# Kernel tuning notes

Hardware: AMD Instinct MI355X
Metric: run time of the kernel (lower is better)

Reference implementation:

```python
import math
import jax, jax.numpy as jnp
import numpy as np

B, T, N_EMBD, N_HEAD = 1, 16384, 1024, 1
N_ITERS = 30


def setup_inputs() -> dict:
    key = jax.random.key(0)
    kx, kw = jax.random.split(key)
    x = jax.random.normal(kx, (B, T, N_EMBD), dtype=jnp.float32)
    W = jax.random.normal(kw, (2 * N_EMBD + 1, N_EMBD), dtype=jnp.float32) * 0.02
    alpha = jnp.asarray(1.0, dtype=jnp.float32)  # nn.Parameter init
    beta = jnp.asarray(5.0, dtype=jnp.float32)   # nn.Parameter init
    return {"x": x, "W": W, "alpha": alpha, "beta": beta}


def _forward(x, W, alpha, beta):
    Bv, Tv, C = x.shape
    hd = C // N_HEAD
    qkv = x @ W.T                                            # (B,T,2C+1)
    q, k, v = qkv[..., :C], qkv[..., C:2 * C], qkv[..., 2 * C:]
    kh = k.reshape(Bv, Tv, N_HEAD, hd).transpose(0, 2, 1, 3)  # (B,H,T,hd)
    vh = v.reshape(Bv, Tv, N_HEAD, 1).transpose(0, 2, 1, 3)   # (B,H,T,1)
    q_last = q[:, -1].reshape(Bv, N_HEAD, hd)                 # last-token query
    scale = 0.001 / math.sqrt(hd)
    # Only the last query row of the causal attention matrix is consumed;
    # it attends all T keys (causal mask is all-ones on the last row).
    att = jnp.einsum('bhd,bhtd->bht', q_last, kh) * scale     # (B,H,T)
    att = att.at[:, :, -1].set(-jnp.inf)                      # exclude self key
    idx = jnp.arange(Tv)
    counts = (Tv - 1 - idx).astype(att.dtype)                 # distance from end

    def step(carry, _):
        a, b, k_old, done, p = carry
        kk = 2.0 * (a + b) / a                                # truncated window k = 2/p
        window = jnp.ceil(kk)
        mask = idx >= (Tv - window)                           # last `window` keys
        p_new = jax.nn.softmax(jnp.where(mask, att, -jnp.inf), axis=-1)
        bu = jnp.einsum('bht,t->', p_new, counts)             # beta_update (B=H=1 -> scalar)
        a_new, b_new = a + 1.0, b + bu
        done_new = done | (kk > Tv) | (kk < k_old)            # torch break conditions
        k_old_new = jax.lax.stop_gradient(kk)                 # k_old = k.detach()
        keep = lambda old, new: jnp.where(done, old, new)     # freeze after break
        return (keep(a, a_new), keep(b, b_new), keep(k_old, k_old_new),
                done_new, keep(p, p_new)), None

    init = (alpha.astype(att.dtype), beta.astype(att.dtype),
            jnp.asarray(0.0, att.dtype), jnp.asarray(False), jnp.zeros_like(att))
    (_, _, _, _, p), _ = jax.lax.scan(step, init, None, length=N_ITERS)
    # p is zero outside the final window, so the full-length contraction equals
    # att @ v[:, :, -window:, :].
    y = jnp.einsum('bht,bhtd->bhd', p, vh)
    return y.reshape(Bv, 1, 1)


def reference(x, W, alpha, beta):
    return _forward(x, W, alpha, beta)
```

## Files before the change

### kernel.cpp

```cpp
#include <hip/hip_runtime.h>
#include <math.h>

#define T_LEN 16384
#define C_DIM 1024
#define TAIL  256
#define SCAN_ITERS 30
#define NBLK 128
#define NTHR 512
#define ROWS_PER_BLK 8
#define ATT_PER_BLK  (TAIL / NBLK)

__global__ __launch_bounds__(NTHR)
void k_fused(const float* __restrict__ x, const float* __restrict__ W,
             const float* __restrict__ alpha_p, const float* __restrict__ beta_p,
             unsigned int* __restrict__ cnt, float* __restrict__ partials,
             float* __restrict__ att, float* __restrict__ v,
             float* __restrict__ out) {
    const int tid = threadIdx.x, lane = tid & 63, wid = tid >> 6;
    const int blk = blockIdx.x;

    __shared__ float q_sh[ROWS_PER_BLK];
    __shared__ float w_sh[C_DIM];
    __shared__ float redA[8], redV[8];
    __shared__ float red4[4];
    __shared__ float totZ[4], totC[4], totV[4];
    __shared__ float sZ[TAIL], sV[TAIL], sBU[TAIL];
    __shared__ int   last_sh;

    {
        const float4* xl = (const float4*)(x + (size_t)(T_LEN - 1) * C_DIM);
        const int i = blk * ROWS_PER_BLK + wid;
        const float4* wq = (const float4*)(W + (size_t)i * C_DIM);
        float acc = 0.f;
#pragma unroll
        for (int it = 0; it < 4; ++it) {
            float4 a = wq[lane + 64 * it];
            float4 b = xl[lane + 64 * it];
            acc += a.x * b.x + a.y * b.y + a.z * b.z + a.w * b.w;
        }
#pragma unroll
        for (int off = 32; off > 0; off >>= 1) acc += __shfl_down(acc, off, 64);
        if (lane == 0) q_sh[wid] = acc;
        __syncthreads();

        const float* Wk = W + (size_t)C_DIM * C_DIM;
        float2 p2 = make_float2(0.f, 0.f);
#pragma unroll
        for (int r = 0; r < ROWS_PER_BLK; ++r) {
            int ir = blk * ROWS_PER_BLK + r;
            float2 wkv = ((const float2*)(Wk + (size_t)ir * C_DIM))[tid];
            float qv = q_sh[r];
            p2.x += qv * wkv.x; p2.y += qv * wkv.y;
        }
        ((float2*)(partials + (size_t)blk * C_DIM))[tid] = p2;
    }

    __syncthreads();
    if (tid == 0) {
        __threadfence();
        atomicAdd(&cnt[0], 1u);
        while (__hip_atomic_load(&cnt[0], __ATOMIC_ACQUIRE,
                                 __HIP_MEMORY_SCOPE_AGENT) < NBLK) { }
    }
    __syncthreads();
    __threadfence();

    {
        float2 a2 = make_float2(0.f, 0.f);
        for (int b = 0; b < NBLK; ++b) {
            float2 p = ((const float2*)(partials + (size_t)b * C_DIM))[tid];
            a2.x += p.x; a2.y += p.y;
        }
        w_sh[2 * tid]     = a2.x;
        w_sh[2 * tid + 1] = a2.y;
        __syncthreads();

        const int r = wid >> 2, qt = wid & 3;
        const int gw = blk * ATT_PER_BLK + r;
        const int t  = T_LEN - TAIL + gw;
        const float4* xr  = (const float4*)(x + (size_t)t * C_DIM);
        const float4* ws4 = (const float4*)w_sh;
        const float4* wv  = (const float4*)(W + (size_t)(2 * C_DIM) * C_DIM);
        const int idx = qt * 64 + lane;
        float4 a  = xr[idx];
        float4 e  = ws4[idx];
        float4 bv = wv[idx];
        float accA = a.x * e.x  + a.y * e.y  + a.z * e.z  + a.w * e.w;
        float accV = a.x * bv.x + a.y * bv.y + a.z * bv.z + a.w * bv.w;
#pragma unroll
        for (int off = 32; off > 0; off >>= 1) {
            accA += __shfl_down(accA, off, 64);
            accV += __shfl_down(accV, off, 64);
        }
        if (lane == 0) { redA[wid] = accA; redV[wid] = accV; }
        __syncthreads();
        if (tid < ATT_PER_BLK) {
            float A = redA[4 * tid] + redA[4 * tid + 1] + redA[4 * tid + 2] + redA[4 * tid + 3];
            float V = redV[4 * tid] + redV[4 * tid + 1] + redV[4 * tid + 2] + redV[4 * tid + 3];
            int gw2 = blk * ATT_PER_BLK + tid;
            int t2  = T_LEN - TAIL + gw2;
            const float scale = (float)(0.001 / 32.0);
            att[gw2] = (t2 == T_LEN - 1) ? -INFINITY : A * scale;
            v[gw2]   = V;
        }
    }

    __syncthreads();
    if (tid == 0) {
        __threadfence();
        unsigned int ticket = atomicAdd(&cnt[1], 1u);
        last_sh = (ticket == NBLK - 1);
    }
    __syncthreads();
    if (!last_sh) return;
    __threadfence();

    const int u = TAIL - 1 - tid;
    float av = -INFINITY, vv = 0.f;
    if (tid < TAIL) { av = att[u]; vv = v[u]; }

    float m = av;
#pragma unroll
    for (int off = 32; off > 0; off >>= 1) m = fmaxf(m, __shfl_xor(m, off, 64));
    if (lane == 0 && wid < 4) red4[wid] = m;
    __syncthreads();
    m = fmaxf(fmaxf(red4[0], red4[1]), fmaxf(red4[2], red4[3]));

    float e = (tid < TAIL) ? expf(av - m) : 0.f;
    float c = e * (float)(TAIL - 1 - u);
    float w = e * vv;

    float pz = e, pc = c, pw = w;
#pragma unroll
    for (int off = 1; off < 64; off <<= 1) {
        float tz = __shfl_up(pz, off, 64);
        float tc = __shfl_up(pc, off, 64);
        float tw = __shfl_up(pw, off, 64);
        if (lane >= off) { pz += tz; pc += tc; pw += tw; }
    }
    if (lane == 63 && wid < 4) { totZ[wid] = pz; totC[wid] = pc; totV[wid] = pw; }
    __syncthreads();
    if (tid < TAIL) {
        float az = 0.f, ac = 0.f, aw = 0.f;
        for (int w2 = 0; w2 < wid; ++w2) { az += totZ[w2]; ac += totC[w2]; aw += totV[w2]; }
        float Zu = pz + az;
        sZ[u]  = Zu;
        sV[u]  = pw + aw;
        sBU[u] = (pc + ac) / Zu;
    }
    __syncthreads();

    if (tid == 0) {
        float a = alpha_p[0], b = beta_p[0], k_old = 0.f;
        int f_start = 0;
        for (int it = 0; it < SCAN_ITERS; ++it) {
            float kk = 2.0f * (a + b) / a;
            float wf = ceilf(kk);
            int start;
            if (wf >= (float)TAIL) start = 0;
            else { int win = (int)wf; start = TAIL - win; if (start < 0) start = 0; }

            float bu = sBU[start];
            f_start = start;
            bool done_next = (kk > (float)T_LEN) || (kk < k_old);
            k_old = kk;
            a += 1.0f;
            b += bu;
            if (done_next) break;
        }
        out[0] = sV[f_start] / sZ[f_start];
    }
}

extern "C" void kernel_launch(void* const* d_in, const int* in_sizes, int n_in,
                              void* d_out, int out_size, void* d_ws, size_t ws_size,
                              hipStream_t stream) {
    const float* x     = (const float*)d_in[0];
    const float* W     = (const float*)d_in[1];
    const float* alpha = (const float*)d_in[2];
    const float* beta  = (const float*)d_in[3];

    unsigned int* cnt = (unsigned int*)d_ws;
    float* ws         = (float*)d_ws;
    float* partials   = ws + 16;
    float* att        = partials + (size_t)NBLK * C_DIM;
    float* v          = att + TAIL;
    float* outp       = (float*)d_out;

    hipMemsetAsync(cnt, 0, 2 * sizeof(unsigned int), stream);
    k_fused<<<NBLK, NTHR, 0, stream>>>(x, W, alpha, beta, cnt,
                                       partials, att, v, outp);
}
```

Measured before the change: 133.9 us.

## Double grid size and distribute partial-sum reduction across blocks with extra grid barrier

Grid grows from 128 to 256 blocks, each handling 4 query rows (split across two half-waves) and one tail attention row. The reduction of per-block partials into the effective key vector, which every block used to repeat over all partials, is now split across 64 blocks and written to a shared buffer, followed by a second grid-wide spin barrier. Spin-waits use relaxed loads with s_sleep. This is meant to cut redundant partials reading and spread the q and W_k load over more CUs, at the cost of an extra global barrier and of relying on all 256 blocks being co-resident.

```diff
diff --git a/kernel.cpp b/kernel.cpp
--- a/kernel.cpp
+++ b/kernel.cpp
@@ -5,22 +5,23 @@
 #define C_DIM 1024
 #define TAIL  256
 #define SCAN_ITERS 30
-#define NBLK 128
+#define NBLK 256
 #define NTHR 512
-#define ROWS_PER_BLK 8
-#define ATT_PER_BLK  (TAIL / NBLK)
+#define ROWS_PER_BLK 4
+#define NRED 64
 
 __global__ __launch_bounds__(NTHR)
 void k_fused(const float* __restrict__ x, const float* __restrict__ W,
              const float* __restrict__ alpha_p, const float* __restrict__ beta_p,
-             unsigned int* __restrict__ cnt, float* __restrict__ partials,
+             unsigned int* __restrict__ cnt, float* __restrict__ w_eff,
              float* __restrict__ att, float* __restrict__ v,
-             float* __restrict__ out) {
+             float* __restrict__ partials, float* __restrict__ out) {
     const int tid = threadIdx.x, lane = tid & 63, wid = tid >> 6;
     const int blk = blockIdx.x;
 
+    __shared__ float qp[8];
     __shared__ float q_sh[ROWS_PER_BLK];
-    __shared__ float w_sh[C_DIM];
+    __shared__ float red2[8 * 16];
     __shared__ float redA[8], redV[8];
     __shared__ float red4[4];
     __shared__ float totZ[4], totC[4], totV[4];
@@ -28,28 +29,32 @@
     __shared__ int   last_sh;
 
     {
+        const int r = wid & 3, h = wid >> 2;
+        const int i = blk * ROWS_PER_BLK + r;
         const float4* xl = (const float4*)(x + (size_t)(T_LEN - 1) * C_DIM);
-        const int i = blk * ROWS_PER_BLK + wid;
         const float4* wq = (const float4*)(W + (size_t)i * C_DIM);
         float acc = 0.f;
 #pragma unroll
-        for (int it = 0; it < 4; ++it) {
-            float4 a = wq[lane + 64 * it];
-            float4 b = xl[lane + 64 * it];
+        for (int it = 0; it < 2; ++it) {
+            int idx = h * 128 + it * 64 + lane;
+            float4 a = wq[idx];
+            float4 b = xl[idx];
             acc += a.x * b.x + a.y * b.y + a.z * b.z + a.w * b.w;
         }
 #pragma unroll
         for (int off = 32; off > 0; off >>= 1) acc += __shfl_down(acc, off, 64);
-        if (lane == 0) q_sh[wid] = acc;
+        if (lane == 0) qp[wid] = acc;
+        __syncthreads();
+        if (tid < ROWS_PER_BLK) q_sh[tid] = qp[tid] + qp[tid + 4];
         __syncthreads();
 
         const float* Wk = W + (size_t)C_DIM * C_DIM;
         float2 p2 = make_float2(0.f, 0.f);
 #pragma unroll
-        for (int r = 0; r < ROWS_PER_BLK; ++r) {
-            int ir = blk * ROWS_PER_BLK + r;
+        for (int r2 = 0; r2 < ROWS_PER_BLK; ++r2) {
+            int ir = blk * ROWS_PER_BLK + r2;
             float2 wkv = ((const float2*)(Wk + (size_t)ir * C_DIM))[tid];
-            float qv = q_sh[r];
+            float qv = q_sh[r2];
             p2.x += qv * wkv.x; p2.y += qv * wkv.y;
         }
         ((float2*)(partials + (size_t)blk * C_DIM))[tid] = p2;
@@ -59,34 +64,53 @@
     if (tid == 0) {
         __threadfence();
         atomicAdd(&cnt[0], 1u);
-        while (__hip_atomic_load(&cnt[0], __ATOMIC_ACQUIRE,
-                                 __HIP_MEMORY_SCOPE_AGENT) < NBLK) { }
+        while (__hip_atomic_load(&cnt[0], __ATOMIC_RELAXED,
+                                 __HIP_MEMORY_SCOPE_AGENT) < NBLK)
+            __builtin_amdgcn_s_sleep(2);
     }
     __syncthreads();
     __threadfence();
 
+    if (blk < NRED) {
+        const int cl = tid & 15, rt = tid >> 4;
+        const int c = blk * 16 + cl;
+        float s = 0.f;
+#pragma unroll
+        for (int rr = 0; rr < 8; ++rr)
+            s += partials[(size_t)(rt + 32 * rr) * C_DIM + c];
+        s += __shfl_down(s, 32, 64);
+        s += __shfl_down(s, 16, 64);
+        if ((lane >> 4) == 0) red2[wid * 16 + cl] = s;
+        __syncthreads();
+        if (tid < 16) {
+            float t2 = 0.f;
+#pragma unroll
+            for (int w2 = 0; w2 < 8; ++w2) t2 += red2[w2 * 16 + tid];
+            w_eff[blk * 16 + tid] = t2;
+        }
+        __syncthreads();
+    }
+
+    if (tid == 0) {
+        __threadfence();
+        atomicAdd(&cnt[1], 1u);
+        while (__hip_atomic_load(&cnt[1], __ATOMIC_RELAXED,
+                                 __HIP_MEMORY_SCOPE_AGENT) < NBLK)
+            __builtin_amdgcn_s_sleep(2);
+    }
+    __syncthreads();
+    __threadfence();
+
     {
-        float2 a2 = make_float2(0.f, 0.f);
-        for (int b = 0; b < NBLK; ++b) {
-            float2 p = ((const float2*)(partials + (size_t)b * C_DIM))[tid];
-            a2.x += p.x; a2.y += p.y;
-        }
-        w_sh[2 * tid]     = a2.x;
-        w_sh[2 * tid + 1] = a2.y;
-        __syncthreads();
-
-        const int r = wid >> 2, qt = wid & 3;
-        const int gw = blk * ATT_PER_BLK + r;
-        const int t  = T_LEN - TAIL + gw;
-        const float4* xr  = (const float4*)(x + (size_t)t * C_DIM);
-        const float4* ws4 = (const float4*)w_sh;
-        const float4* wv  = (const float4*)(W + (size_t)(2 * C_DIM) * C_DIM);
-        const int idx = qt * 64 + lane;
-        float4 a  = xr[idx];
-        float4 e  = ws4[idx];
-        float4 bv = wv[idx];
-        float accA = a.x * e.x  + a.y * e.y  + a.z * e.z  + a.w * e.w;
-        float accV = a.x * bv.x + a.y * bv.y + a.z * bv.z + a.w * bv.w;
+        const int t = T_LEN - TAIL + blk;
+        const float2* xr  = (const float2*)(x + (size_t)t * C_DIM);
+        const float2* we2 = (const float2*)w_eff;
+        const float2* wv2 = (const float2*)(W + (size_t)(2 * C_DIM) * C_DIM);
+        float2 a  = xr[tid];
+        float2 e  = we2[tid];
+        float2 bv = wv2[tid];
+        float accA = a.x * e.x  + a.y * e.y;
+        float accV = a.x * bv.x + a.y * bv.y;
 #pragma unroll
         for (int off = 32; off > 0; off >>= 1) {
             accA += __shfl_down(accA, off, 64);
@@ -94,21 +118,20 @@
         }
         if (lane == 0) { redA[wid] = accA; redV[wid] = accV; }
         __syncthreads();
-        if (tid < ATT_PER_BLK) {
-            float A = redA[4 * tid] + redA[4 * tid + 1] + redA[4 * tid + 2] + redA[4 * tid + 3];
-            float V = redV[4 * tid] + redV[4 * tid + 1] + redV[4 * tid + 2] + redV[4 * tid + 3];
-            int gw2 = blk * ATT_PER_BLK + tid;
-            int t2  = T_LEN - TAIL + gw2;
+        if (tid == 0) {
+            float A = 0.f, V = 0.f;
+#pragma unroll
+            for (int w2 = 0; w2 < 8; ++w2) { A += redA[w2]; V += redV[w2]; }
             const float scale = (float)(0.001 / 32.0);
-            att[gw2] = (t2 == T_LEN - 1) ? -INFINITY : A * scale;
-            v[gw2]   = V;
+            att[blk] = (t == T_LEN - 1) ? -INFINITY : A * scale;
+            v[blk]   = V;
         }
     }
 
     __syncthreads();
     if (tid == 0) {
         __threadfence();
-        unsigned int ticket = atomicAdd(&cnt[1], 1u);
+        unsigned int ticket = atomicAdd(&cnt[2], 1u);
         last_sh = (ticket == NBLK - 1);
     }
     __syncthreads();
@@ -180,14 +203,15 @@
     const float* alpha = (const float*)d_in[2];
     const float* beta  = (const float*)d_in[3];
 
+    float* ws         = (float*)d_ws;
     unsigned int* cnt = (unsigned int*)d_ws;
-    float* ws         = (float*)d_ws;
-    float* partials   = ws + 16;
-    float* att        = partials + (size_t)NBLK * C_DIM;
+    float* w_eff      = ws + 16;
+    float* att        = w_eff + C_DIM;
     float* v          = att + TAIL;
+    float* partials   = v + TAIL;
     float* outp       = (float*)d_out;
 
-    hipMemsetAsync(cnt, 0, 2 * sizeof(unsigned int), stream);
+    hipMemsetAsync(cnt, 0, 4 * sizeof(unsigned int), stream);
     k_fused<<<NBLK, NTHR, 0, stream>>>(x, W, alpha, beta, cnt,
-                                       partials, att, v, outp);
+                                       w_eff, att, v, partials, outp);
 }
```

Result: slower. 191.4 us (+42.9%).

## Split fused kernel into three launches replacing grid-wide spin barrier

Applied to the files above, without the earlier changes.

The single fused kernel with a software grid barrier is replaced by three kernels: a partial q·Wk projection, a column reduction of partials across 64 blocks, and an att/v kernel that finishes the scan in the last block. The counter reset moves into the reduction kernel, so the separate memset launch goes away. This is meant to remove the spin-wait barrier and the serial 128-way partial reduction that every block repeated. In exchange it adds kernel launch boundaries, and the partial buffer grows to 256 rows.

```diff
diff --git a/kernel.cpp b/kernel.cpp
--- a/kernel.cpp
+++ b/kernel.cpp
@@ -5,86 +5,89 @@
 #define C_DIM 1024
 #define TAIL  256
 #define SCAN_ITERS 30
-#define NBLK 128
-#define NTHR 512
-#define ROWS_PER_BLK 8
-#define ATT_PER_BLK  (TAIL / NBLK)
 
-__global__ __launch_bounds__(NTHR)
-void k_fused(const float* __restrict__ x, const float* __restrict__ W,
-             const float* __restrict__ alpha_p, const float* __restrict__ beta_p,
-             unsigned int* __restrict__ cnt, float* __restrict__ partials,
-             float* __restrict__ att, float* __restrict__ v,
-             float* __restrict__ out) {
+
+__global__ __launch_bounds__(256)
+void k_qw(const float* __restrict__ x, const float* __restrict__ W,
+          float* __restrict__ partials) {
     const int tid = threadIdx.x, lane = tid & 63, wid = tid >> 6;
     const int blk = blockIdx.x;
+    __shared__ float q_sh[4];
 
-    __shared__ float q_sh[ROWS_PER_BLK];
-    __shared__ float w_sh[C_DIM];
-    __shared__ float redA[8], redV[8];
+    const float4* xl = (const float4*)(x + (size_t)(T_LEN - 1) * C_DIM);
+    const int row = blk * 4 + wid;
+    const float4* wq = (const float4*)(W + (size_t)row * C_DIM);
+    float acc = 0.f;
+#pragma unroll
+    for (int it = 0; it < 4; ++it) {
+        int idx = lane + 64 * it;
+        float4 a = wq[idx];
+        float4 b = xl[idx];
+        acc += a.x * b.x + a.y * b.y + a.z * b.z + a.w * b.w;
+    }
+#pragma unroll
+    for (int off = 32; off > 0; off >>= 1) acc += __shfl_down(acc, off, 64);
+    if (lane == 0) q_sh[wid] = acc;
+    __syncthreads();
+
+    const float* Wk = W + (size_t)C_DIM * C_DIM;
+    float4 p4 = make_float4(0.f, 0.f, 0.f, 0.f);
+#pragma unroll
+    for (int r = 0; r < 4; ++r) {
+        int ir = blk * 4 + r;
+        float4 wkv = ((const float4*)(Wk + (size_t)ir * C_DIM))[tid];
+        float qv = q_sh[r];
+        p4.x += qv * wkv.x; p4.y += qv * wkv.y;
+        p4.z += qv * wkv.z; p4.w += qv * wkv.w;
+    }
+    ((float4*)(partials + (size_t)blk * C_DIM))[tid] = p4;
+}
+
+__global__ __launch_bounds__(256)
+void k_red(const float* __restrict__ partials, float* __restrict__ w_eff,
+           unsigned int* __restrict__ cnt) {
+    const int tid = threadIdx.x, blk = blockIdx.x;
+    if (blk == 0 && tid == 0) cnt[0] = 0;
+    __shared__ float sh[16][17];
+    const int cl = tid & 15, seg = tid >> 4;
+    const int col = blk * 16 + cl;
+    float s = 0.f;
+#pragma unroll
+    for (int r = 0; r < 16; ++r)
+        s += partials[(size_t)(seg * 16 + r) * C_DIM + col];
+    sh[seg][cl] = s;
+    __syncthreads();
+    if (tid < 16) {
+        float t2 = 0.f;
+#pragma unroll
+        for (int g = 0; g < 16; ++g) t2 += sh[g][tid];
+        w_eff[blk * 16 + tid] = t2;
+    }
+}
+
+__global__ __launch_bounds__(256)
+void k_attv(const float* __restrict__ x, const float* __restrict__ W,
+            const float* __restrict__ w_eff,
+            const float* __restrict__ alpha_p, const float* __restrict__ beta_p,
+            unsigned int* __restrict__ cnt,
+            float* __restrict__ att, float* __restrict__ v,
+            float* __restrict__ out) {
+    const int tid = threadIdx.x, lane = tid & 63, wid = tid >> 6;
+    const int blk = blockIdx.x;
+    __shared__ float redA[4], redV[4];
     __shared__ float red4[4];
     __shared__ float totZ[4], totC[4], totV[4];
     __shared__ float sZ[TAIL], sV[TAIL], sBU[TAIL];
     __shared__ int   last_sh;
 
     {
-        const float4* xl = (const float4*)(x + (size_t)(T_LEN - 1) * C_DIM);
-        const int i = blk * ROWS_PER_BLK + wid;
-        const float4* wq = (const float4*)(W + (size_t)i * C_DIM);
-        float acc = 0.f;
-#pragma unroll
-        for (int it = 0; it < 4; ++it) {
-            float4 a = wq[lane + 64 * it];
-            float4 b = xl[lane + 64 * it];
-            acc += a.x * b.x + a.y * b.y + a.z * b.z + a.w * b.w;
-        }
-#pragma unroll
-        for (int off = 32; off > 0; off >>= 1) acc += __shfl_down(acc, off, 64);
-        if (lane == 0) q_sh[wid] = acc;
-        __syncthreads();
-
-        const float* Wk = W + (size_t)C_DIM * C_DIM;
-        float2 p2 = make_float2(0.f, 0.f);
-#pragma unroll
-        for (int r = 0; r < ROWS_PER_BLK; ++r) {
-            int ir = blk * ROWS_PER_BLK + r;
-            float2 wkv = ((const float2*)(Wk + (size_t)ir * C_DIM))[tid];
-            float qv = q_sh[r];
-            p2.x += qv * wkv.x; p2.y += qv * wkv.y;
-        }
-        ((float2*)(partials + (size_t)blk * C_DIM))[tid] = p2;
-    }
-
-    __syncthreads();
-    if (tid == 0) {
-        __threadfence();
-        atomicAdd(&cnt[0], 1u);
-        while (__hip_atomic_load(&cnt[0], __ATOMIC_ACQUIRE,
-                                 __HIP_MEMORY_SCOPE_AGENT) < NBLK) { }
-    }
-    __syncthreads();
-    __threadfence();
-
-    {
-        float2 a2 = make_float2(0.f, 0.f);
-        for (int b = 0; b < NBLK; ++b) {
-            float2 p = ((const float2*)(partials + (size_t)b * C_DIM))[tid];
-            a2.x += p.x; a2.y += p.y;
-        }
-        w_sh[2 * tid]     = a2.x;
-        w_sh[2 * tid + 1] = a2.y;
-        __syncthreads();
-
-        const int r = wid >> 2, qt = wid & 3;
-        const int gw = blk * ATT_PER_BLK + r;
-        const int t  = T_LEN - TAIL + gw;
-        const float4* xr  = (const float4*)(x + (size_t)t * C_DIM);
-        const float4* ws4 = (const float4*)w_sh;
-        const float4* wv  = (const float4*)(W + (size_t)(2 * C_DIM) * C_DIM);
-        const int idx = qt * 64 + lane;
-        float4 a  = xr[idx];
-        float4 e  = ws4[idx];
-        float4 bv = wv[idx];
+        const int t = T_LEN - TAIL + blk;
+        const float4* xr = (const float4*)(x + (size_t)t * C_DIM);
+        const float4* we = (const float4*)w_eff;
+        const float4* wv = (const float4*)(W + (size_t)(2 * C_DIM) * C_DIM);
+        float4 a  = xr[tid];
+        float4 e  = we[tid];
+        float4 bv = wv[tid];
         float accA = a.x * e.x  + a.y * e.y  + a.z * e.z  + a.w * e.w;
         float accV = a.x * bv.x + a.y * bv.y + a.z * bv.z + a.w * bv.w;
 #pragma unroll
@@ -94,39 +97,37 @@
         }
         if (lane == 0) { redA[wid] = accA; redV[wid] = accV; }
         __syncthreads();
-        if (tid < ATT_PER_BLK) {
-            float A = redA[4 * tid] + redA[4 * tid + 1] + redA[4 * tid + 2] + redA[4 * tid + 3];
-            float V = redV[4 * tid] + redV[4 * tid + 1] + redV[4 * tid + 2] + redV[4 * tid + 3];
-            int gw2 = blk * ATT_PER_BLK + tid;
-            int t2  = T_LEN - TAIL + gw2;
+        if (tid == 0) {
+            float A = redA[0] + redA[1] + redA[2] + redA[3];
+            float V = redV[0] + redV[1] + redV[2] + redV[3];
             const float scale = (float)(0.001 / 32.0);
-            att[gw2] = (t2 == T_LEN - 1) ? -INFINITY : A * scale;
-            v[gw2]   = V;
+            att[blk] = (t == T_LEN - 1) ? -INFINITY : A * scale;
+            v[blk]   = V;
         }
     }
 
     __syncthreads();
     if (tid == 0) {
         __threadfence();
-        unsigned int ticket = atomicAdd(&cnt[1], 1u);
-        last_sh = (ticket == NBLK - 1);
+        unsigned int ticket = atomicAdd(&cnt[0], 1u);
+        last_sh = (ticket == 255u);
     }
     __syncthreads();
     if (!last_sh) return;
     __threadfence();
 
     const int u = TAIL - 1 - tid;
-    float av = -INFINITY, vv = 0.f;
-    if (tid < TAIL) { av = att[u]; vv = v[u]; }
+    const float av = att[u];
+    const float vv = v[u];
 
     float m = av;
 #pragma unroll
     for (int off = 32; off > 0; off >>= 1) m = fmaxf(m, __shfl_xor(m, off, 64));
-    if (lane == 0 && wid < 4) red4[wid] = m;
+    if (lane == 0) red4[wid] = m;
     __syncthreads();
     m = fmaxf(fmaxf(red4[0], red4[1]), fmaxf(red4[2], red4[3]));
 
-    float e = (tid < TAIL) ? expf(av - m) : 0.f;
+    float e = expf(av - m);
     float c = e * (float)(TAIL - 1 - u);
     float w = e * vv;
 
@@ -138,9 +139,9 @@
         float tw = __shfl_up(pw, off, 64);
         if (lane >= off) { pz += tz; pc += tc; pw += tw; }
     }
-    if (lane == 63 && wid < 4) { totZ[wid] = pz; totC[wid] = pc; totV[wid] = pw; }
+    if (lane == 63) { totZ[wid] = pz; totC[wid] = pc; totV[wid] = pw; }
     __syncthreads();
-    if (tid < TAIL) {
+    {
         float az = 0.f, ac = 0.f, aw = 0.f;
         for (int w2 = 0; w2 < wid; ++w2) { az += totZ[w2]; ac += totC[w2]; aw += totV[w2]; }
         float Zu = pz + az;
@@ -180,14 +181,15 @@
     const float* alpha = (const float*)d_in[2];
     const float* beta  = (const float*)d_in[3];
 
+    float* ws         = (float*)d_ws;
     unsigned int* cnt = (unsigned int*)d_ws;
-    float* ws         = (float*)d_ws;
-    float* partials   = ws + 16;
-    float* att        = partials + (size_t)NBLK * C_DIM;
+    float* w_eff      = ws + 16;
+    float* att        = w_eff + C_DIM;
     float* v          = att + TAIL;
+    float* partials   = v + TAIL;
     float* outp       = (float*)d_out;
 
-    hipMemsetAsync(cnt, 0, 2 * sizeof(unsigned int), stream);
-    k_fused<<<NBLK, NTHR, 0, stream>>>(x, W, alpha, beta, cnt,
-                                       partials, att, v, outp);
+    k_qw  <<<256, 256, 0, stream>>>(x, W, partials);
+    k_red <<<64,  256, 0, stream>>>(partials, w_eff, cnt);
+    k_attv<<<256, 256, 0, stream>>>(x, W, w_eff, alpha, beta, cnt, att, v, outp);
 }
```

Result: faster. 108.9 us (median of 2 runs) (-18.7%).
